# Kernel optimization log

Hardware: AMD Instinct MI355X
Metric: run time of the kernel (lower is better)

The kernel has to match this reference:

```python
import jax, jax.numpy as jnp
import numpy as np

T = 2097152          # total points across all diagrams (per side)
N_DGM = 256          # number of diagrams
D_IN, D_HID, D_OUT = 2, 32, 32


def setup_inputs() -> dict:
    key = jax.random.key(0)
    ks = jax.random.split(key, 12)
    s = 0.3
    inp = {
        "points_t": jax.random.normal(ks[0], (T, D_IN), jnp.float32),
        "points_s": jax.random.normal(ks[1], (T, D_IN), jnp.float32),
        "w1_w": jax.random.normal(ks[2], (D_IN, D_HID), jnp.float32) * s,
        "w1_b": jax.random.normal(ks[3], (D_HID,), jnp.float32) * s,
        "w2_w": jax.random.normal(ks[4], (D_HID, 1), jnp.float32) * s,
        "w2_b": jax.random.normal(ks[5], (1,), jnp.float32) * s,
        "e1_w": jax.random.normal(ks[6], (D_IN, D_HID), jnp.float32) * s,
        "e1_b": jax.random.normal(ks[7], (D_HID,), jnp.float32) * s,
        "e2_w": jax.random.normal(ks[8], (D_HID, D_OUT), jnp.float32) * s,
        "e2_b": jax.random.normal(ks[9], (D_OUT,), jnp.float32) * s,
        "seg_t": jnp.sort(jax.random.randint(ks[10], (T,), 0, N_DGM, jnp.int32)),
        "seg_s": jnp.sort(jax.random.randint(ks[11], (T,), 0, N_DGM, jnp.int32)),
        "num_diagrams": N_DGM,
    }
    return inp


def _point_pool(pts, seg, w1_w, w1_b, w2_w, w2_b, e1_w, e1_b, e2_w, e2_b, n_dgm):
    # torch.nan_to_num(dgm, posinf=0)
    x = jnp.nan_to_num(pts, posinf=0.0)
    # weight MLP: Linear(2,32) -> ReLU -> Linear(32,1)
    w = jax.nn.relu(x @ w1_w + w1_b) @ w2_w + w2_b            # [T, 1]
    # embedding MLP: Linear(2,32) -> ReLU -> Linear(32,32)
    e = jax.nn.relu(x @ e1_w + e1_b) @ e2_w + e2_b            # [T, 32]
    prod = w * e                                              # [T, 32]
    sums = jax.ops.segment_sum(prod, seg, num_segments=n_dgm)               # [N, 32]
    cnts = jax.ops.segment_sum(jnp.ones((pts.shape[0], 1), prod.dtype), seg,
                               num_segments=n_dgm)                          # [N, 1]
    pooled = sums / jnp.maximum(cnts, 1.0)                    # per-diagram mean
    return pooled.reshape(-1)                                 # torch.cat -> [N*32]


def reference(points_t, points_s, w1_w, w1_b, w2_w, w2_b, e1_w, e1_b, e2_w, e2_b,
              seg_t, seg_s, num_diagrams):
    params = (w1_w, w1_b, w2_w, w2_b, e1_w, e1_b, e2_w, e2_b)
    emb_t = _point_pool(points_t, seg_t, *params, num_diagrams)
    emb_s = _point_pool(points_s, seg_s, *params, num_diagrams)
    return jnp.mean((emb_s - emb_t) ** 2)
```

## Files before the change

kernel.cpp:

```cpp
#include <hip/hip_runtime.h>

typedef float f4 __attribute__((ext_vector_type(4)));

#define NSEG 256
#define BPS 2
#define KPT 8
#define NSLOT 8
#define STRIDE (BPS * 256 * KPT)


__global__ __launch_bounds__(256) void bounds2_kernel(
    const int* __restrict__ seg_t, const int* __restrict__ seg_s,
    int* __restrict__ starts_t, int* __restrict__ starts_s, int T) {
  const int side = blockIdx.y;
  const int* seg = side ? seg_s : seg_t;
  int* starts = side ? starts_s : starts_t;
  const int gi = ((int)blockIdx.x * 256 + (int)threadIdx.x) * 16;
  if (gi >= T) return;
  const int4* v = (const int4*)(seg + gi);
  const int4 a = v[0], b = v[1], c = v[2], d = v[3];
  const int s[16] = {a.x, a.y, a.z, a.w, b.x, b.y, b.z, b.w,
                     c.x, c.y, c.z, c.w, d.x, d.y, d.z, d.w};
  int prev = (gi == 0) ? -1 : seg[gi - 1];
#pragma unroll
  for (int k = 0; k < 16; ++k) {
    for (int t = prev + 1; t <= s[k]; ++t) starts[t] = gi + k;
    prev = s[k];
  }
  if (gi + 16 >= T) {
    for (int t = prev + 1; t <= NSEG; ++t) starts[t] = T;
  }
}

__global__ __launch_bounds__(256, 4) void pool_kernel(
    const float2* __restrict__ pts_t, const float2* __restrict__ pts_s,
    const int* __restrict__ starts_t, const int* __restrict__ starts_s,
    const float* __restrict__ w1_w, const float* __restrict__ w1_b,
    const float* __restrict__ w2_w, const float* __restrict__ w2_b,
    const float* __restrict__ e1_w, const float* __restrict__ e1_b,
    float* __restrict__ part_g, float* __restrict__ part_w, int T) {
  const int side = blockIdx.z;
  const float2* pts = side ? pts_s : pts_t;
  const int* starts = side ? starts_s : starts_t;
  const int s = blockIdx.x;
  const int tid = threadIdx.x;

  __shared__ __align__(16) float wtA[8][16];
  __shared__ __align__(16) float wtB[8][12];
  __shared__ float w2b_sh;
  if (tid < 32) {
    const int q = tid >> 2, j = tid & 3, h = tid;
    wtA[q][j] = w1_w[h];
    wtA[q][4 + j] = w1_w[32 + h];
    wtA[q][8 + j] = w1_b[h];
    wtA[q][12 + j] = w2_w[h];
    wtB[q][j] = e1_w[h];
    wtB[q][4 + j] = e1_w[32 + h];
    wtB[q][8 + j] = e1_b[h];
  }
  if (tid == 0) w2b_sh = w2_b[0];
  __syncthreads();

  const int st = starts[s];
  const int en = starts[s + 1];
  const int st2 = st & ~1;
  const int total2 = en - st2;
  const int Tm2 = T - 2;
  const unsigned cnt = (unsigned)(en - st);
  const float w2b = w2b_sh;

  float ag[32];
#pragma unroll
  for (int h = 0; h < 32; ++h) ag[h] = 0.f;
  float aw = 0.f;

  for (int base = ((int)blockIdx.y * 256 + tid) * KPT; base < total2;
       base += STRIDE) {
    const int i0 = st2 + base;

    float px[KPT], py[KPT];
#pragma unroll
    for (int j = 0; j < 4; ++j) {
      int ip = i0 + 2 * j;
      ip = ip > Tm2 ? Tm2 : ip;
      const f4 q = *reinterpret_cast<const f4*>(&pts[ip]);
      px[2 * j] = q.x;
      py[2 * j] = q.y;
      px[2 * j + 1] = q.z;
      py[2 * j + 1] = q.w;
    }

    unsigned zoff = 0;
    asm volatile("" : "+v"(zoff));
    const char* wa = (const char*)(&wtA[0][0]) + zoff;
    const char* wbp = (const char*)(&wtB[0][0]) + zoff;

    float wacc[KPT];
#pragma unroll
    for (int k = 0; k < KPT; ++k) wacc[k] = 0.f;

#pragma unroll
    for (int q = 0; q < 8; ++q) {
      const f4 QX = *(const f4*)(wa + q * 64);
      const f4 QY = *(const f4*)(wa + q * 64 + 16);
      const f4 QB = *(const f4*)(wa + q * 64 + 32);
      const f4 QW = *(const f4*)(wa + q * 64 + 48);
#pragma unroll
      for (int k = 0; k < KPT; ++k) {
        float h0 = fmaf(px[k], QX.x, fmaf(py[k], QY.x, QB.x));
        wacc[k] = fmaf(fmaxf(h0, 0.f), QW.x, wacc[k]);
        float h1 = fmaf(px[k], QX.y, fmaf(py[k], QY.y, QB.y));
        wacc[k] = fmaf(fmaxf(h1, 0.f), QW.y, wacc[k]);
        float h2 = fmaf(px[k], QX.z, fmaf(py[k], QY.z, QB.z));
        wacc[k] = fmaf(fmaxf(h2, 0.f), QW.z, wacc[k]);
        float h3 = fmaf(px[k], QX.w, fmaf(py[k], QY.w, QB.w));
        wacc[k] = fmaf(fmaxf(h3, 0.f), QW.w, wacc[k]);
      }
    }

    float wv[KPT];
#pragma unroll
    for (int k = 0; k < KPT; ++k) {
      float w = wacc[k] + w2b;
      const bool valid = (unsigned)(i0 + k - st) < cnt;
      w = valid ? w : 0.f;
      wv[k] = w;
      aw += w;
    }

#pragma unroll
    for (int q = 0; q < 8; ++q) {
      const f4 EX = *(const f4*)(wbp + q * 48);
      const f4 EY = *(const f4*)(wbp + q * 48 + 16);
      const f4 EB = *(const f4*)(wbp + q * 48 + 32);
      float a0 = ag[4 * q], a1 = ag[4 * q + 1];
      float a2 = ag[4 * q + 2], a3 = ag[4 * q + 3];
#pragma unroll
      for (int k = 0; k < KPT; ++k) {
        const float e0 = fmaxf(fmaf(px[k], EX.x, fmaf(py[k], EY.x, EB.x)), 0.f);
        a0 = fmaf(wv[k], e0, a0);
        const float e1 = fmaxf(fmaf(px[k], EX.y, fmaf(py[k], EY.y, EB.y)), 0.f);
        a1 = fmaf(wv[k], e1, a1);
        const float e2 = fmaxf(fmaf(px[k], EX.z, fmaf(py[k], EY.z, EB.z)), 0.f);
        a2 = fmaf(wv[k], e2, a2);
        const float e3 = fmaxf(fmaf(px[k], EX.w, fmaf(py[k], EY.w, EB.w)), 0.f);
        a3 = fmaf(wv[k], e3, a3);
      }
      ag[4 * q] = a0;
      ag[4 * q + 1] = a1;
      ag[4 * q + 2] = a2;
      ag[4 * q + 3] = a3;
    }
  }

  float v[32];
#pragma unroll
  for (int h = 0; h < 32; ++h) v[h] = ag[h];
  const int l = tid & 63;

#define FOLD(M, HALF)                                    \
  {                                                      \
    const bool hi = (l & (M)) != 0;                      \
    _Pragma("unroll") for (int i = 0; i < (HALF); ++i) { \
      const float sent = hi ? v[i] : v[i + (HALF)];      \
      const float kept = hi ? v[i + (HALF)] : v[i];      \
      v[i] = kept + __shfl_xor(sent, (M));               \
    }                                                    \
  }
  FOLD(1, 16)
  FOLD(2, 8)
  FOLD(4, 4)
  FOLD(8, 2)
  FOLD(16, 1)
#undef FOLD
  v[0] += __shfl_xor(v[0], 32);
  const int h = ((l & 1) << 4) | ((l & 2) << 2) | (l & 4) | ((l & 8) >> 2) |
                ((l & 16) >> 4);

#pragma unroll
  for (int m = 1; m < 64; m <<= 1) aw += __shfl_xor(aw, m);

  const int slot = (int)blockIdx.y * 4 + (tid >> 6);
  const int unit = side * NSEG + s;
  if (l < 32) part_g[(unit * NSLOT + slot) * 32 + h] = v[0];
  if (l == 0) part_w[unit * NSLOT + slot] = aw;
}

__global__ __launch_bounds__(256) void finishA_kernel(
    const float* __restrict__ part_g, const float* __restrict__ part_w,
    float* __restrict__ emb_g, float* __restrict__ emb_w) {
  const int gu = blockIdx.x * 8 + (threadIdx.x >> 5);
  const int h = threadIdx.x & 31;
  const float* pg = part_g + gu * NSLOT * 32 + h;
  float sum = 0.f;
#pragma unroll
  for (int k = 0; k < NSLOT; ++k) sum += pg[k * 32];
  emb_g[gu * 32 + h] = sum;
  if (h == 0) {
    const float* pw = part_w + gu * NSLOT;
    float sw = 0.f;
#pragma unroll
    for (int k = 0; k < NSLOT; ++k) sw += pw[k];
    emb_w[gu] = sw;
  }
}

__global__ __launch_bounds__(256) void finishB_kernel(
    const float* __restrict__ emb_g, const float* __restrict__ emb_w,
    const int* __restrict__ starts_t, const int* __restrict__ starts_s,
    const float* __restrict__ e2_w, const float* __restrict__ e2_b,
    float* __restrict__ out) {
  const int s = threadIdx.x;
  __shared__ float e2s[32][33];
  __shared__ float e2bs[32];
  for (int k = threadIdx.x; k < 1024; k += 256) e2s[k >> 5][k & 31] = e2_w[k];
  if (threadIdx.x < 32) e2bs[threadIdx.x] = e2_b[threadIdx.x];
  __syncthreads();

  const float* gt = &emb_g[s * 32];
  const float* gs = &emb_g[(NSEG + s) * 32];
  const float awt = emb_w[s];
  const float aws = emb_w[NSEG + s];
  const float ct = fmaxf((float)(starts_t[s + 1] - starts_t[s]), 1.f);
  const float cs = fmaxf((float)(starts_s[s + 1] - starts_s[s]), 1.f);

  float gtl[32], gsl[32];
#pragma unroll
  for (int h = 0; h < 32; ++h) {
    gtl[h] = gt[h];
    gsl[h] = gs[h];
  }

  float part = 0.f;
#pragma unroll
  for (int o = 0; o < 32; ++o) {
    float pt = awt * e2bs[o];
    float ps = aws * e2bs[o];
#pragma unroll
    for (int h = 0; h < 32; ++h) {
      const float w = e2s[h][o];
      pt = fmaf(gtl[h], w, pt);
      ps = fmaf(gsl[h], w, ps);
    }
    pt /= ct;
    ps /= cs;
    const float d = ps - pt;
    part = fmaf(d, d, part);
  }

  __shared__ float red[256];
  red[threadIdx.x] = part;
  __syncthreads();
  for (int k = 128; k > 0; k >>= 1) {
    if (threadIdx.x < k) red[threadIdx.x] += red[threadIdx.x + k];
    __syncthreads();
  }
  if (threadIdx.x == 0) out[0] = red[0] / (float)(NSEG * 32);
}

extern "C" void kernel_launch(void* const* d_in, const int* in_sizes, int n_in,
                              void* d_out, int out_size, void* d_ws,
                              size_t ws_size, hipStream_t stream) {
  const float2* pts_t = (const float2*)d_in[0];
  const float2* pts_s = (const float2*)d_in[1];
  const float* w1_w = (const float*)d_in[2];
  const float* w1_b = (const float*)d_in[3];
  const float* w2_w = (const float*)d_in[4];
  const float* w2_b = (const float*)d_in[5];
  const float* e1_w = (const float*)d_in[6];
  const float* e1_b = (const float*)d_in[7];
  const float* e2_w = (const float*)d_in[8];
  const float* e2_b = (const float*)d_in[9];
  const int* seg_t = (const int*)d_in[10];
  const int* seg_s = (const int*)d_in[11];
  const int T = in_sizes[0] / 2;

  char* ws = (char*)d_ws;
  int* starts_t = (int*)ws;
  int* starts_s = (int*)(ws + 1028);
  float* part_g = (float*)(ws + 4096);
  float* part_w = (float*)(ws + 528384);
  float* emb_g = (float*)(ws + 544768);
  float* emb_w = (float*)(ws + 610304);

  dim3 gA((T / 16 + 255) / 256, 2, 1);
  bounds2_kernel<<<gA, 256, 0, stream>>>(seg_t, seg_s, starts_t, starts_s, T);

  dim3 gB(NSEG, BPS, 2);
  pool_kernel<<<gB, 256, 0, stream>>>(pts_t, pts_s, starts_t, starts_s, w1_w,
                                      w1_b, w2_w, w2_b, e1_w, e1_b, part_g,
                                      part_w, T);

  finishA_kernel<<<64, 256, 0, stream>>>(part_g, part_w, emb_g, emb_w);
  finishB_kernel<<<1, 256, 0, stream>>>(emb_g, emb_w, starts_t, starts_s, e2_w,
                                        e2_b, (float*)d_out);
}
```

Before: 50.26 us.

## Split weight-MLP into separate flat-parallel kernel, stream weights to segmented pool

Splits the fused pooling kernel in two. A new kernel computes the per-point scalar weight MLP over all points, indexed flat and independent of segments, and writes it to a workspace buffer. The segmented pool kernel then reloads those weights instead of recomputing them, and now runs 3 blocks per segment with a 4-aligned start. This is meant to improve occupancy and balance the ALU-heavy weight MLP across the GPU. The cost is an extra kernel launch, 16 MB of extra global writes and reads, and a second read of the points.

```diff
diff --git a/kernel.cpp b/kernel.cpp
--- a/kernel.cpp
+++ b/kernel.cpp
@@ -3,10 +3,10 @@
 typedef float f4 __attribute__((ext_vector_type(4)));
 
 #define NSEG 256
-#define BPS 2
+#define BPS 3
 #define KPT 8
-#define NSLOT 8
-#define STRIDE (BPS * 256 * KPT)
+#define NSLOT 12
+#define STRIDE_E (BPS * 256 * KPT)
 
 
 __global__ __launch_bounds__(256) void bounds2_kernel(
@@ -32,21 +32,17 @@
   }
 }
 
-__global__ __launch_bounds__(256, 4) void pool_kernel(
+__global__ __launch_bounds__(256, 8) void poolW_kernel(
     const float2* __restrict__ pts_t, const float2* __restrict__ pts_s,
-    const int* __restrict__ starts_t, const int* __restrict__ starts_s,
     const float* __restrict__ w1_w, const float* __restrict__ w1_b,
     const float* __restrict__ w2_w, const float* __restrict__ w2_b,
-    const float* __restrict__ e1_w, const float* __restrict__ e1_b,
-    float* __restrict__ part_g, float* __restrict__ part_w, int T) {
-  const int side = blockIdx.z;
+    float* __restrict__ wv, int T) {
+  const int side = blockIdx.y;
   const float2* pts = side ? pts_s : pts_t;
-  const int* starts = side ? starts_s : starts_t;
-  const int s = blockIdx.x;
+  float* wvs = wv + (size_t)side * T;
   const int tid = threadIdx.x;
 
   __shared__ __align__(16) float wtA[8][16];
-  __shared__ __align__(16) float wtB[8][12];
   __shared__ float w2b_sh;
   if (tid < 32) {
     const int q = tid >> 2, j = tid & 3, h = tid;
@@ -54,29 +50,102 @@
     wtA[q][4 + j] = w1_w[32 + h];
     wtA[q][8 + j] = w1_b[h];
     wtA[q][12 + j] = w2_w[h];
+  }
+  if (tid == 0) w2b_sh = w2_b[0];
+  __syncthreads();
+
+  const int base = ((int)blockIdx.x * 256 + tid) * KPT;
+  if (base >= T) return;
+  const int Tm2 = T - 2;
+
+  float px[KPT], py[KPT];
+#pragma unroll
+  for (int j = 0; j < 4; ++j) {
+    int ip = base + 2 * j;
+    ip = ip > Tm2 ? Tm2 : ip;
+    const f4 q = *reinterpret_cast<const f4*>(&pts[ip]);
+    px[2 * j] = q.x;
+    py[2 * j] = q.y;
+    px[2 * j + 1] = q.z;
+    py[2 * j + 1] = q.w;
+  }
+
+  unsigned zoff = 0;
+  asm volatile("" : "+v"(zoff));
+  const char* wa = (const char*)(&wtA[0][0]) + zoff;
+
+  float wacc[KPT];
+#pragma unroll
+  for (int k = 0; k < KPT; ++k) wacc[k] = 0.f;
+
+#pragma unroll
+  for (int q = 0; q < 8; ++q) {
+    const f4 QX = *(const f4*)(wa + q * 64);
+    const f4 QY = *(const f4*)(wa + q * 64 + 16);
+    const f4 QB = *(const f4*)(wa + q * 64 + 32);
+    const f4 QW = *(const f4*)(wa + q * 64 + 48);
+#pragma unroll
+    for (int k = 0; k < KPT; ++k) {
+      float h0 = fmaf(px[k], QX.x, fmaf(py[k], QY.x, QB.x));
+      wacc[k] = fmaf(fmaxf(h0, 0.f), QW.x, wacc[k]);
+      float h1 = fmaf(px[k], QX.y, fmaf(py[k], QY.y, QB.y));
+      wacc[k] = fmaf(fmaxf(h1, 0.f), QW.y, wacc[k]);
+      float h2 = fmaf(px[k], QX.z, fmaf(py[k], QY.z, QB.z));
+      wacc[k] = fmaf(fmaxf(h2, 0.f), QW.z, wacc[k]);
+      float h3 = fmaf(px[k], QX.w, fmaf(py[k], QY.w, QB.w));
+      wacc[k] = fmaf(fmaxf(h3, 0.f), QW.w, wacc[k]);
+    }
+  }
+
+  const float w2b = w2b_sh;
+  if (base + KPT <= T) {
+    f4 o0 = {wacc[0] + w2b, wacc[1] + w2b, wacc[2] + w2b, wacc[3] + w2b};
+    f4 o1 = {wacc[4] + w2b, wacc[5] + w2b, wacc[6] + w2b, wacc[7] + w2b};
+    *reinterpret_cast<f4*>(&wvs[base]) = o0;
+    *reinterpret_cast<f4*>(&wvs[base + 4]) = o1;
+  } else {
+    for (int k = 0; base + k < T; ++k) wvs[base + k] = wacc[k] + w2b;
+  }
+}
+
+__global__ __launch_bounds__(256, 6) void poolE_kernel(
+    const float2* __restrict__ pts_t, const float2* __restrict__ pts_s,
+    const int* __restrict__ starts_t, const int* __restrict__ starts_s,
+    const float* __restrict__ e1_w, const float* __restrict__ e1_b,
+    const float* __restrict__ wv, float* __restrict__ part_g,
+    float* __restrict__ part_w, int T) {
+  const int side = blockIdx.z;
+  const float2* pts = side ? pts_s : pts_t;
+  const int* starts = side ? starts_s : starts_t;
+  const float* wvs = wv + (size_t)side * T;
+  const int s = blockIdx.x;
+  const int tid = threadIdx.x;
+
+  __shared__ __align__(16) float wtB[8][12];
+  if (tid < 32) {
+    const int q = tid >> 2, j = tid & 3, h = tid;
     wtB[q][j] = e1_w[h];
     wtB[q][4 + j] = e1_w[32 + h];
     wtB[q][8 + j] = e1_b[h];
   }
-  if (tid == 0) w2b_sh = w2_b[0];
   __syncthreads();
 
   const int st = starts[s];
   const int en = starts[s + 1];
-  const int st2 = st & ~1;
-  const int total2 = en - st2;
+  const int st4 = st & ~3;
+  const int total4 = en - st4;
   const int Tm2 = T - 2;
+  const int Tm4 = T - 4;
   const unsigned cnt = (unsigned)(en - st);
-  const float w2b = w2b_sh;
 
   float ag[32];
 #pragma unroll
   for (int h = 0; h < 32; ++h) ag[h] = 0.f;
   float aw = 0.f;
 
-  for (int base = ((int)blockIdx.y * 256 + tid) * KPT; base < total2;
-       base += STRIDE) {
-    const int i0 = st2 + base;
+  for (int base = ((int)blockIdx.y * 256 + tid) * KPT; base < total4;
+       base += STRIDE_E) {
+    const int i0 = st4 + base;
 
     float px[KPT], py[KPT];
 #pragma unroll
@@ -90,43 +159,21 @@
       py[2 * j + 1] = q.w;
     }
 
+    int iw0 = i0 > Tm4 ? Tm4 : i0;
+    int iw1 = i0 + 4 > Tm4 ? Tm4 : i0 + 4;
+    const f4 wa4 = *reinterpret_cast<const f4*>(&wvs[iw0]);
+    const f4 wb4 = *reinterpret_cast<const f4*>(&wvs[iw1]);
+    float wvl[KPT] = {wa4.x, wa4.y, wa4.z, wa4.w, wb4.x, wb4.y, wb4.z, wb4.w};
+#pragma unroll
+    for (int k = 0; k < KPT; ++k) {
+      const bool valid = (unsigned)(i0 + k - st) < cnt;
+      wvl[k] = valid ? wvl[k] : 0.f;
+      aw += wvl[k];
+    }
+
     unsigned zoff = 0;
     asm volatile("" : "+v"(zoff));
-    const char* wa = (const char*)(&wtA[0][0]) + zoff;
     const char* wbp = (const char*)(&wtB[0][0]) + zoff;
-
-    float wacc[KPT];
-#pragma unroll
-    for (int k = 0; k < KPT; ++k) wacc[k] = 0.f;
-
-#pragma unroll
-    for (int q = 0; q < 8; ++q) {
-      const f4 QX = *(const f4*)(wa + q * 64);
-      const f4 QY = *(const f4*)(wa + q * 64 + 16);
-      const f4 QB = *(const f4*)(wa + q * 64 + 32);
-      const f4 QW = *(const f4*)(wa + q * 64 + 48);
-#pragma unroll
-      for (int k = 0; k < KPT; ++k) {
-        float h0 = fmaf(px[k], QX.x, fmaf(py[k], QY.x, QB.x));
-        wacc[k] = fmaf(fmaxf(h0, 0.f), QW.x, wacc[k]);
-        float h1 = fmaf(px[k], QX.y, fmaf(py[k], QY.y, QB.y));
-        wacc[k] = fmaf(fmaxf(h1, 0.f), QW.y, wacc[k]);
-        float h2 = fmaf(px[k], QX.z, fmaf(py[k], QY.z, QB.z));
-        wacc[k] = fmaf(fmaxf(h2, 0.f), QW.z, wacc[k]);
-        float h3 = fmaf(px[k], QX.w, fmaf(py[k], QY.w, QB.w));
-        wacc[k] = fmaf(fmaxf(h3, 0.f), QW.w, wacc[k]);
-      }
-    }
-
-    float wv[KPT];
-#pragma unroll
-    for (int k = 0; k < KPT; ++k) {
-      float w = wacc[k] + w2b;
-      const bool valid = (unsigned)(i0 + k - st) < cnt;
-      w = valid ? w : 0.f;
-      wv[k] = w;
-      aw += w;
-    }
 
 #pragma unroll
     for (int q = 0; q < 8; ++q) {
@@ -138,13 +185,13 @@
 #pragma unroll
       for (int k = 0; k < KPT; ++k) {
         const float e0 = fmaxf(fmaf(px[k], EX.x, fmaf(py[k], EY.x, EB.x)), 0.f);
-        a0 = fmaf(wv[k], e0, a0);
+        a0 = fmaf(wvl[k], e0, a0);
         const float e1 = fmaxf(fmaf(px[k], EX.y, fmaf(py[k], EY.y, EB.y)), 0.f);
-        a1 = fmaf(wv[k], e1, a1);
+        a1 = fmaf(wvl[k], e1, a1);
         const float e2 = fmaxf(fmaf(px[k], EX.z, fmaf(py[k], EY.z, EB.z)), 0.f);
-        a2 = fmaf(wv[k], e2, a2);
+        a2 = fmaf(wvl[k], e2, a2);
         const float e3 = fmaxf(fmaf(px[k], EX.w, fmaf(py[k], EY.w, EB.w)), 0.f);
-        a3 = fmaf(wv[k], e3, a3);
+        a3 = fmaf(wvl[k], e3, a3);
       }
       ag[4 * q] = a0;
       ag[4 * q + 1] = a1;
@@ -278,18 +325,22 @@
   char* ws = (char*)d_ws;
   int* starts_t = (int*)ws;
   int* starts_s = (int*)(ws + 1028);
-  float* part_g = (float*)(ws + 4096);
-  float* part_w = (float*)(ws + 528384);
-  float* emb_g = (float*)(ws + 544768);
-  float* emb_w = (float*)(ws + 610304);
+  float* wvb = (float*)(ws + 4096);
+  float* part_g = (float*)(ws + 16781312);
+  float* part_w = (float*)(ws + 17567744);
+  float* emb_g = (float*)(ws + 17592320);
+  float* emb_w = (float*)(ws + 17657856);
 
   dim3 gA((T / 16 + 255) / 256, 2, 1);
   bounds2_kernel<<<gA, 256, 0, stream>>>(seg_t, seg_s, starts_t, starts_s, T);
 
-  dim3 gB(NSEG, BPS, 2);
-  pool_kernel<<<gB, 256, 0, stream>>>(pts_t, pts_s, starts_t, starts_s, w1_w,
-                                      w1_b, w2_w, w2_b, e1_w, e1_b, part_g,
-                                      part_w, T);
+  dim3 gW((T + 256 * KPT - 1) / (256 * KPT), 2, 1);
+  poolW_kernel<<<gW, 256, 0, stream>>>(pts_t, pts_s, w1_w, w1_b, w2_w, w2_b,
+                                       wvb, T);
+
+  dim3 gE(NSEG, BPS, 2);
+  poolE_kernel<<<gE, 256, 0, stream>>>(pts_t, pts_s, starts_t, starts_s, e1_w,
+                                       e1_b, wvb, part_g, part_w, T);
 
   finishA_kernel<<<64, 256, 0, stream>>>(part_g, part_w, emb_g, emb_w);
   finishB_kernel<<<1, 256, 0, stream>>>(emb_g, emb_w, starts_t, starts_s, e2_w,
```

Result: slower. 176.2 us (+250.5%).
